# Kernel optimization log

Hardware: AMD Instinct MI355X
Metric: run time of the kernel (lower is better)

Reference implementation:

```python
import jax, jax.numpy as jnp
import numpy as np

MAX_LEN = 200
MAX_K = 3
ITERATION = 3
NEG_PAD = -2.0 ** 16 + 1.0


def setup_inputs() -> dict:
    key = jax.random.key(0)
    k1, k2, k3, k4 = jax.random.split(key, 4)
    B, L, D_in, D_out = 1024, MAX_LEN, 128, 128
    low_capsule = jax.random.normal(k1, (B, L, D_in), dtype=jnp.float32)
    B_matrix = jax.random.normal(k2, (1, MAX_K, L), dtype=jnp.float32)
    S_matrix = jax.random.normal(k3, (D_in, D_out), dtype=jnp.float32)
    # lengths in [1, MAX_LEN]; at least one row hits MAX_LEN so max(seq_len)==MAX_LEN
    seq_len = jax.random.randint(k4, (B, 1), 1, MAX_LEN + 1, dtype=jnp.int64)
    seq_len = seq_len.at[0, 0].set(MAX_LEN)
    return {"low_capsule": low_capsule, "B_matrix": B_matrix,
            "S_matrix": S_matrix, "seq_len": seq_len}


def squash(x):
    # torch code: norm over dim=1 (the capsule axis), keepdim
    sq = jnp.sum(jnp.square(x), axis=1, keepdims=True)
    scale = sq / (1.0 + sq) / jnp.sqrt(sq + 1e-9)
    return scale * x


def reference(low_capsule, B_matrix, S_matrix, seq_len):
    # low_capsule: [B, L, D_in], B_matrix: [1, K, L], S_matrix: [D_in, D_out], seq_len: [B, 1]
    # mask: [B, K, L] (seq_len tiled over K via broadcasting)
    mask = jnp.arange(MAX_LEN)[None, None, :] < seq_len[:, :, None]
    # bilinear projection is loop-invariant (same math as recomputing each iter)
    low_new = jnp.einsum('bld,de->ble', low_capsule, S_matrix)  # [B, L, D_out]
    high = None
    for _ in range(ITERATION):
        logits = jnp.where(mask, B_matrix, jnp.float32(NEG_PAD))  # [B, K, L]
        W = jax.nn.softmax(logits, axis=-1)
        high = squash(jnp.einsum('bkl,ble->bke', W, low_new))  # [B, K, D_out]
        # agreement, summed over batch with keepdim -> [1, K, L]
        B_delta = jnp.einsum('bke,ble->kl', high, low_new)[None]
        B_matrix = B_matrix + B_delta
    return high
```

## Files before the change

### kernel.cpp

```cpp
#include <hip/hip_runtime.h>
#include <math.h>

#define BATCH 1024
#define SEQ   200
#define DIN   128
#define DOUT  128
#define PSTR  608

typedef __attribute__((ext_vector_type(8))) short short8;
typedef __attribute__((ext_vector_type(4))) float f32x4;

__device__ __forceinline__ void async_copy16(const void* g, void* l) {
    __builtin_amdgcn_global_load_lds((const __attribute__((address_space(1))) void*)g,
                                     (__attribute__((address_space(3))) void*)l,
                                     16, 0, 0);
}

__device__ __forceinline__ void split2(float f, short& h, short& l) {
    unsigned u = __float_as_uint(f);
    unsigned r = u + 0x8000u;
    h = (short)(r >> 16);
    float hf = __uint_as_float(r & 0xffff0000u);
    l = (short)(__float_as_uint(f - hf) >> 16);
}

__global__ __launch_bounds__(256) void k_presplit(const float* __restrict__ S,
                                                  short* __restrict__ Sp) {
    int g = blockIdx.x * 256 + threadIdx.x;
    int j = g & 7, lane = (g >> 3) & 63, kt = (g >> 9) & 3, nt = g >> 11;
    int k = kt * 32 + (lane >> 4) * 8 + j;
    int n = nt * 16 + (lane & 15);
    short h, l;
    split2(S[k * DOUT + n], h, l);
    Sp[g] = h;
    Sp[16384 + g] = l;
}

__global__ __launch_bounds__(256, 4) void k_gemm(const float* __restrict__ A,
                                                 const short* __restrict__ Sp,
                                                 float* __restrict__ outn) {
    __shared__ short sSp[16384];
    const int t = threadIdx.x;
    const int w = t >> 6, lane = t & 63;
    const int q = lane >> 4, c = lane & 15;
    const int cg = blockIdx.x & 1;
    const long rowb = (long)(blockIdx.x >> 1) * 128 + w * 32;

    float4 araw[4][2][2];
#pragma unroll
    for (int kt = 0; kt < 4; ++kt)
#pragma unroll
        for (int mt = 0; mt < 2; ++mt) {
            const float* ap = A + (rowb + mt * 16 + c) * DIN + kt * 32 + q * 8;
            araw[kt][mt][0] = *(const float4*)ap;
            araw[kt][mt][1] = *(const float4*)(ap + 4);
        }

#pragma unroll
    for (int i = 0; i < 4; ++i) {
        const int g = w * 4 + i;
        async_copy16(Sp + cg * 8192 + g * 512 + lane * 8, &sSp[g * 512]);
        async_copy16(Sp + 16384 + cg * 8192 + g * 512 + lane * 8, &sSp[8192 + g * 512]);
    }

    short8 ah[4][2], al[4][2];
#pragma unroll
    for (int kt = 0; kt < 4; ++kt)
#pragma unroll
        for (int mt = 0; mt < 2; ++mt) {
            float av[8];
            *(float4*)&av[0] = araw[kt][mt][0];
            *(float4*)&av[4] = araw[kt][mt][1];
#pragma unroll
            for (int j = 0; j < 8; ++j) {
                short h, l;
                split2(av[j], h, l);
                ah[kt][mt][j] = h; al[kt][mt][j] = l;
            }
        }

    f32x4 acc[2][4];
    const f32x4 zz = {0.f, 0.f, 0.f, 0.f};
#pragma unroll
    for (int mt = 0; mt < 2; ++mt)
#pragma unroll
        for (int nt = 0; nt < 4; ++nt) acc[mt][nt] = zz;

    __syncthreads();

#pragma unroll
    for (int kt = 0; kt < 4; ++kt)
#pragma unroll
        for (int nt = 0; nt < 4; ++nt) {
            const int fo = ((nt * 4 + kt) * 64 + lane) * 8;
            short8 sh = *(const short8*)&sSp[fo];
            short8 sl = *(const short8*)&sSp[8192 + fo];
#pragma unroll
            for (int mt = 0; mt < 2; ++mt) {
                acc[mt][nt] = __builtin_amdgcn_mfma_f32_16x16x32_bf16(ah[kt][mt], sh, acc[mt][nt], 0, 0, 0);
                acc[mt][nt] = __builtin_amdgcn_mfma_f32_16x16x32_bf16(al[kt][mt], sh, acc[mt][nt], 0, 0, 0);
                acc[mt][nt] = __builtin_amdgcn_mfma_f32_16x16x32_bf16(ah[kt][mt], sl, acc[mt][nt], 0, 0, 0);
            }
        }
#pragma unroll
    for (int mt = 0; mt < 2; ++mt)
#pragma unroll
        for (int nt = 0; nt < 4; ++nt) {
            const long r0 = rowb + mt * 16 + q * 4;
            const int col = cg * 64 + nt * 16 + c;
#pragma unroll
            for (int r = 0; r < 4; ++r)
                outn[(r0 + r) * DOUT + col] = acc[mt][nt][r];
        }
}

__global__ __launch_bounds__(256, 4) void k_iter(
    const float* __restrict__ lown,
    const float* __restrict__ Bm,
    const int* __restrict__ seq,
    const float* __restrict__ acc0, const float* __restrict__ acc1,
    float* __restrict__ part,
    float* __restrict__ out, int iter) {
    __shared__ float sW[3][SEQ];
    __shared__ f32x4 pBf[815];
    __shared__ float sH[3][64];

    const int t = threadIdx.x, lane = t & 63;
    const int m = t >> 4, cg = t & 15;
    const int b = blockIdx.x >> 1, half = blockIdx.x & 1;
    const float* lp = lown + (size_t)b * (SEQ * DIN) + half * 64;

    float4 dat[13];
#pragma unroll
    for (int i = 0; i < 13; ++i) {
        int r = m + 16 * i;
        int rc = (r < SEQ) ? r : SEQ - 1;
        dat[i] = *(const float4*)(lp + rc * DIN + cg * 4);
    }

    const int n = seq[b];
#pragma unroll
    for (int k = 0; k < 3; ++k) {
        float vv[4], mx = -INFINITY;
#pragma unroll
        for (int i2 = 0; i2 < 4; ++i2) {
            int l = lane + 64 * i2;
            float v = -INFINITY;
            if (l < n) {
                v = Bm[k * SEQ + l];
                if (iter >= 1) v += acc0[k * SEQ + l];
                if (iter >= 2) v += acc1[k * SEQ + l];
            }
            vv[i2] = v;
            mx = fmaxf(mx, v);
        }
        for (int off = 32; off; off >>= 1) mx = fmaxf(mx, __shfl_xor(mx, off, 64));
        float s = 0.f, pv[4];
#pragma unroll
        for (int i2 = 0; i2 < 4; ++i2) {
            pv[i2] = (vv[i2] == -INFINITY) ? 0.f : expf(vv[i2] - mx);
            s += pv[i2];
        }
        for (int off = 32; off; off >>= 1) s += __shfl_xor(s, off, 64);
        float rs = 1.f / s;
#pragma unroll
        for (int i2 = 0; i2 < 4; ++i2) {
            int l = lane + 64 * i2;
            if (l < SEQ) sW[k][l] = pv[i2] * rs;
        }
    }

    f32x4 h0 = {0.f, 0.f, 0.f, 0.f}, h1 = h0, h2 = h0;
#pragma unroll
    for (int i = 0; i < 13; ++i) {
        int r = m + 16 * i;
        if (r < SEQ) {
            float w0 = sW[0][r], w1 = sW[1][r], w2 = sW[2][r];
            f32x4 f = {dat[i].x, dat[i].y, dat[i].z, dat[i].w};
            h0 += w0 * f; h1 += w1 * f; h2 += w2 * f;
        }
    }
    pBf[(m * 3 + 0) * 17 + cg] = h0;
    pBf[(m * 3 + 1) * 17 + cg] = h1;
    pBf[(m * 3 + 2) * 17 + cg] = h2;
    __syncthreads();

    if (t < 64) {
        const int ecg = t >> 2, ej = t & 3;
        float g0 = 0.f, g1 = 0.f, g2 = 0.f;
#pragma unroll
        for (int mm = 0; mm < 16; ++mm) {
            g0 += pBf[(mm * 3 + 0) * 17 + ecg][ej];
            g1 += pBf[(mm * 3 + 1) * 17 + ecg][ej];
            g2 += pBf[(mm * 3 + 2) * 17 + ecg][ej];
        }
        float sq = g0 * g0 + g1 * g1 + g2 * g2;
        float scale = sq / (1.f + sq) / sqrtf(sq + 1e-9f);
        g0 *= scale; g1 *= scale; g2 *= scale;
        if (iter == 2) {
            size_t o = (size_t)b * 3 * DOUT + half * 64 + t;
            out[o] = g0; out[o + DOUT] = g1; out[o + 2 * DOUT] = g2;
        } else {
            sH[0][t] = g0; sH[1][t] = g1; sH[2][t] = g2;
        }
    }
    if (iter == 2) return;
    __syncthreads();

    f32x4 x0 = *(const f32x4*)&sH[0][cg * 4];
    f32x4 x1 = *(const f32x4*)&sH[1][cg * 4];
    f32x4 x2 = *(const f32x4*)&sH[2][cg * 4];
    float* pp = part + (size_t)blockIdx.x * PSTR;
#pragma unroll
    for (int i = 0; i < 13; ++i) {
        int r = m + 16 * i;
        if (r < SEQ) {
            f32x4 f = {dat[i].x, dat[i].y, dat[i].z, dat[i].w};
            f32x4 p0 = x0 * f, p1 = x1 * f, p2 = x2 * f;
            float d0 = p0[0] + p0[1] + p0[2] + p0[3];
            float d1 = p1[0] + p1[1] + p1[2] + p1[3];
            float d2 = p2[0] + p2[1] + p2[2] + p2[3];
#pragma unroll
            for (int off = 1; off < 16; off <<= 1) {
                d0 += __shfl_xor(d0, off, 64);
                d1 += __shfl_xor(d1, off, 64);
                d2 += __shfl_xor(d2, off, 64);
            }
            if (cg == 0) {
                pp[r] = d0; pp[SEQ + r] = d1; pp[2 * SEQ + r] = d2;
            }
        }
    }
}

__global__ __launch_bounds__(256) void k_reduce(const float* __restrict__ part,
                                                float* __restrict__ accN) {
    const int t = threadIdx.x;
    const int r0 = blockIdx.x * 16;
    if (t < 150) {
        float sx = 0.f, sy = 0.f, sz = 0.f, sw = 0.f;
#pragma unroll
        for (int r = 0; r < 16; ++r) {
            float4 v = *(const float4*)&part[(size_t)(r0 + r) * PSTR + t * 4];
            sx += v.x; sy += v.y; sz += v.z; sw += v.w;
        }
        atomicAdd(&accN[4 * t + 0], sx);
        atomicAdd(&accN[4 * t + 1], sy);
        atomicAdd(&accN[4 * t + 2], sz);
        atomicAdd(&accN[4 * t + 3], sw);
    }
}

extern "C" void kernel_launch(void* const* d_in, const int* in_sizes, int n_in,
                              void* d_out, int out_size, void* d_ws, size_t ws_size,
                              hipStream_t stream) {
    const float* low_capsule = (const float*)d_in[0];
    const float* B_matrix    = (const float*)d_in[1];
    const float* S_matrix    = (const float*)d_in[2];
    const int*   seq_len     = (const int*)d_in[3];
    float* out = (float*)d_out;

    float* lown = (float*)d_ws;
    short* Sp   = (short*)(lown + (size_t)BATCH * SEQ * DOUT);
    float* acc0 = (float*)(Sp + 32768);
    float* acc1 = acc0 + 640;
    float* part = acc1 + 640;

    hipMemsetAsync(acc0, 0, 1280 * sizeof(float), stream);

    k_presplit<<<64, 256, 0, stream>>>(S_matrix, Sp);
    k_gemm<<<2 * (BATCH * SEQ) / 128, 256, 0, stream>>>(low_capsule, Sp, lown);

    k_iter<<<2 * BATCH, 256, 0, stream>>>(lown, B_matrix, seq_len, acc0, acc1, part, out, 0);
    k_reduce<<<128, 256, 0, stream>>>(part, acc0);
    k_iter<<<2 * BATCH, 256, 0, stream>>>(lown, B_matrix, seq_len, acc0, acc1, part, out, 1);
    k_reduce<<<128, 256, 0, stream>>>(part, acc1);
    k_iter<<<2 * BATCH, 256, 0, stream>>>(lown, B_matrix, seq_len, acc0, acc1, part, out, 2);
}
```

Baseline: 293.2 us.

## Reassociate projection to skip materializing low_capsule @ S; apply S per batch

Drops the large GEMM that wrote the projected tensor [B,L,128] to workspace. Each iteration now computes W·low on the raw input, multiplies the 3x128 result by S held in shared memory, and projects high back through S^T to get agreement logits. This removes the GEMM and the write and re-read of the large intermediate. In exchange, every block of every iteration reloads S into LDS (64KB) and does a small scalar FMA matvec, and one 512-thread block now covers a whole batch row with occupancy limited by LDS.

Measured after the change: 288.3 us. No clear change (-1.7%).

```diff
diff --git a/kernel.cpp b/kernel.cpp
--- a/kernel.cpp
+++ b/kernel.cpp
@@ -5,130 +5,42 @@
 #define SEQ   200
 #define DIN   128
 #define DOUT  128
+#define SSTR  129
 #define PSTR  608
 
-typedef __attribute__((ext_vector_type(8))) short short8;
 typedef __attribute__((ext_vector_type(4))) float f32x4;
 
-__device__ __forceinline__ void async_copy16(const void* g, void* l) {
-    __builtin_amdgcn_global_load_lds((const __attribute__((address_space(1))) void*)g,
-                                     (__attribute__((address_space(3))) void*)l,
-                                     16, 0, 0);
-}
-
-__device__ __forceinline__ void split2(float f, short& h, short& l) {
-    unsigned u = __float_as_uint(f);
-    unsigned r = u + 0x8000u;
-    h = (short)(r >> 16);
-    float hf = __uint_as_float(r & 0xffff0000u);
-    l = (short)(__float_as_uint(f - hf) >> 16);
-}
-
-__global__ __launch_bounds__(256) void k_presplit(const float* __restrict__ S,
-                                                  short* __restrict__ Sp) {
-    int g = blockIdx.x * 256 + threadIdx.x;
-    int j = g & 7, lane = (g >> 3) & 63, kt = (g >> 9) & 3, nt = g >> 11;
-    int k = kt * 32 + (lane >> 4) * 8 + j;
-    int n = nt * 16 + (lane & 15);
-    short h, l;
-    split2(S[k * DOUT + n], h, l);
-    Sp[g] = h;
-    Sp[16384 + g] = l;
-}
-
-__global__ __launch_bounds__(256, 4) void k_gemm(const float* __restrict__ A,
-                                                 const short* __restrict__ Sp,
-                                                 float* __restrict__ outn) {
-    __shared__ short sSp[16384];
-    const int t = threadIdx.x;
-    const int w = t >> 6, lane = t & 63;
-    const int q = lane >> 4, c = lane & 15;
-    const int cg = blockIdx.x & 1;
-    const long rowb = (long)(blockIdx.x >> 1) * 128 + w * 32;
-
-    float4 araw[4][2][2];
-#pragma unroll
-    for (int kt = 0; kt < 4; ++kt)
-#pragma unroll
-        for (int mt = 0; mt < 2; ++mt) {
-            const float* ap = A + (rowb + mt * 16 + c) * DIN + kt * 32 + q * 8;
-            araw[kt][mt][0] = *(const float4*)ap;
-            araw[kt][mt][1] = *(const float4*)(ap + 4);
-        }
-
-#pragma unroll
-    for (int i = 0; i < 4; ++i) {
-        const int g = w * 4 + i;
-        async_copy16(Sp + cg * 8192 + g * 512 + lane * 8, &sSp[g * 512]);
-        async_copy16(Sp + 16384 + cg * 8192 + g * 512 + lane * 8, &sSp[8192 + g * 512]);
-    }
-
-    short8 ah[4][2], al[4][2];
-#pragma unroll
-    for (int kt = 0; kt < 4; ++kt)
-#pragma unroll
-        for (int mt = 0; mt < 2; ++mt) {
-            float av[8];
-            *(float4*)&av[0] = araw[kt][mt][0];
-            *(float4*)&av[4] = araw[kt][mt][1];
-#pragma unroll
-            for (int j = 0; j < 8; ++j) {
-                short h, l;
-                split2(av[j], h, l);
-                ah[kt][mt][j] = h; al[kt][mt][j] = l;
-            }
-        }
-
-    f32x4 acc[2][4];
-    const f32x4 zz = {0.f, 0.f, 0.f, 0.f};
-#pragma unroll
-    for (int mt = 0; mt < 2; ++mt)
-#pragma unroll
-        for (int nt = 0; nt < 4; ++nt) acc[mt][nt] = zz;
-
-    __syncthreads();
-
-#pragma unroll
-    for (int kt = 0; kt < 4; ++kt)
-#pragma unroll
-        for (int nt = 0; nt < 4; ++nt) {
-            const int fo = ((nt * 4 + kt) * 64 + lane) * 8;
-            short8 sh = *(const short8*)&sSp[fo];
-            short8 sl = *(const short8*)&sSp[8192 + fo];
-#pragma unroll
-            for (int mt = 0; mt < 2; ++mt) {
-                acc[mt][nt] = __builtin_amdgcn_mfma_f32_16x16x32_bf16(ah[kt][mt], sh, acc[mt][nt], 0, 0, 0);
-                acc[mt][nt] = __builtin_amdgcn_mfma_f32_16x16x32_bf16(al[kt][mt], sh, acc[mt][nt], 0, 0, 0);
-                acc[mt][nt] = __builtin_amdgcn_mfma_f32_16x16x32_bf16(ah[kt][mt], sl, acc[mt][nt], 0, 0, 0);
-            }
-        }
-#pragma unroll
-    for (int mt = 0; mt < 2; ++mt)
-#pragma unroll
-        for (int nt = 0; nt < 4; ++nt) {
-            const long r0 = rowb + mt * 16 + q * 4;
-            const int col = cg * 64 + nt * 16 + c;
-#pragma unroll
-            for (int r = 0; r < 4; ++r)
-                outn[(r0 + r) * DOUT + col] = acc[mt][nt][r];
-        }
-}
-
-__global__ __launch_bounds__(256, 4) void k_iter(
-    const float* __restrict__ lown,
+__global__ __launch_bounds__(512, 1) void k_iter(
+    const float* __restrict__ low,
+    const float* __restrict__ S,
     const float* __restrict__ Bm,
     const int* __restrict__ seq,
     const float* __restrict__ acc0, const float* __restrict__ acc1,
     float* __restrict__ part,
     float* __restrict__ out, int iter) {
-    __shared__ float sW[3][SEQ];
-    __shared__ f32x4 pBf[815];
-    __shared__ float sH[3][64];
-
-    const int t = threadIdx.x, lane = t & 63;
-    const int m = t >> 4, cg = t & 15;
-    const int b = blockIdx.x >> 1, half = blockIdx.x & 1;
-    const float* lp = lown + (size_t)b * (SEQ * DIN) + half * 64;
+    __shared__ float sS[128 * SSTR];
+    __shared__ float sW[3 * SEQ];
+    __shared__ f32x4 pY[8][3][32];
+    __shared__ float sY[3 * 128];
+    __shared__ float sHp[3 * 128];
+    __shared__ float sH[3 * 128];
+    __shared__ float sZ[3 * 128];
+
+    const int t = threadIdx.x, lane = t & 63, w = t >> 6;
+    const int m = t >> 5, cg = t & 31;
+    const int b = blockIdx.x;
+    const float* lp = low + (size_t)b * (SEQ * DIN);
+
+    float r0[4], r1[4], r2[4];
+    if (w < 3) {
+#pragma unroll
+        for (int i = 0; i < 4; ++i) {
+            int l = lane + 64 * i; bool inb = l < SEQ;
+            r0[i] = inb ? Bm[w * SEQ + l] : 0.f;
+            r1[i] = (inb && iter >= 1) ? acc0[w * SEQ + l] : 0.f;
+            r2[i] = (inb && iter >= 2) ? acc1[w * SEQ + l] : 0.f;
+        }
+    }
 
     float4 dat[13];
 #pragma unroll
@@ -138,96 +50,133 @@
         dat[i] = *(const float4*)(lp + rc * DIN + cg * 4);
     }
 
-    const int n = seq[b];
-#pragma unroll
-    for (int k = 0; k < 3; ++k) {
-        float vv[4], mx = -INFINITY;
-#pragma unroll
-        for (int i2 = 0; i2 < 4; ++i2) {
-            int l = lane + 64 * i2;
-            float v = -INFINITY;
-            if (l < n) {
-                v = Bm[k * SEQ + l];
-                if (iter >= 1) v += acc0[k * SEQ + l];
-                if (iter >= 2) v += acc1[k * SEQ + l];
-            }
-            vv[i2] = v;
-            mx = fmaxf(mx, v);
+#pragma unroll
+    for (int i = 0; i < 8; ++i) {
+        int g = t + 512 * i;
+        int r = g >> 5, e = (g & 31) * 4;
+        float4 v = *(const float4*)(S + r * DIN + e);
+        sS[r * SSTR + e + 0] = v.x;
+        sS[r * SSTR + e + 1] = v.y;
+        sS[r * SSTR + e + 2] = v.z;
+        sS[r * SSTR + e + 3] = v.w;
+    }
+
+    if (w < 3) {
+        const int n = seq[b];
+        float mx = -INFINITY, vv[4];
+#pragma unroll
+        for (int i = 0; i < 4; ++i) {
+            int l = lane + 64 * i;
+            float v = r0[i] + r1[i] + r2[i];
+            vv[i] = (l < n) ? v : -INFINITY;
+            if (l < n) mx = fmaxf(mx, v);
         }
         for (int off = 32; off; off >>= 1) mx = fmaxf(mx, __shfl_xor(mx, off, 64));
         float s = 0.f, pv[4];
 #pragma unroll
-        for (int i2 = 0; i2 < 4; ++i2) {
-            pv[i2] = (vv[i2] == -INFINITY) ? 0.f : expf(vv[i2] - mx);
-            s += pv[i2];
+        for (int i = 0; i < 4; ++i) {
+            pv[i] = (vv[i] == -INFINITY) ? 0.f : expf(vv[i] - mx);
+            s += pv[i];
         }
         for (int off = 32; off; off >>= 1) s += __shfl_xor(s, off, 64);
         float rs = 1.f / s;
 #pragma unroll
-        for (int i2 = 0; i2 < 4; ++i2) {
-            int l = lane + 64 * i2;
-            if (l < SEQ) sW[k][l] = pv[i2] * rs;
-        }
-    }
-
-    f32x4 h0 = {0.f, 0.f, 0.f, 0.f}, h1 = h0, h2 = h0;
-#pragma unroll
-    for (int i = 0; i < 13; ++i) {
-        int r = m + 16 * i;
-        if (r < SEQ) {
-            float w0 = sW[0][r], w1 = sW[1][r], w2 = sW[2][r];
-            f32x4 f = {dat[i].x, dat[i].y, dat[i].z, dat[i].w};
-            h0 += w0 * f; h1 += w1 * f; h2 += w2 * f;
-        }
-    }
-    pBf[(m * 3 + 0) * 17 + cg] = h0;
-    pBf[(m * 3 + 1) * 17 + cg] = h1;
-    pBf[(m * 3 + 2) * 17 + cg] = h2;
-    __syncthreads();
-
-    if (t < 64) {
-        const int ecg = t >> 2, ej = t & 3;
-        float g0 = 0.f, g1 = 0.f, g2 = 0.f;
-#pragma unroll
-        for (int mm = 0; mm < 16; ++mm) {
-            g0 += pBf[(mm * 3 + 0) * 17 + ecg][ej];
-            g1 += pBf[(mm * 3 + 1) * 17 + ecg][ej];
-            g2 += pBf[(mm * 3 + 2) * 17 + ecg][ej];
-        }
+        for (int i = 0; i < 4; ++i) {
+            int l = lane + 64 * i;
+            if (l < SEQ) sW[w * SEQ + l] = pv[i] * rs;
+        }
+    }
+    __syncthreads();
+
+    {
+        f32x4 h0 = {0.f, 0.f, 0.f, 0.f}, h1 = h0, h2 = h0;
+#pragma unroll
+        for (int i = 0; i < 13; ++i) {
+            int r = m + 16 * i;
+            if (r < SEQ) {
+                float w0 = sW[r], w1 = sW[SEQ + r], w2 = sW[2 * SEQ + r];
+                f32x4 f = {dat[i].x, dat[i].y, dat[i].z, dat[i].w};
+                h0 += w0 * f; h1 += w1 * f; h2 += w2 * f;
+            }
+        }
+#pragma unroll
+        for (int c = 0; c < 4; ++c) {
+            h0[c] += __shfl_xor(h0[c], 32, 64);
+            h1[c] += __shfl_xor(h1[c], 32, 64);
+            h2[c] += __shfl_xor(h2[c], 32, 64);
+        }
+        if (lane < 32) { pY[w][0][cg] = h0; pY[w][1][cg] = h1; pY[w][2][cg] = h2; }
+    }
+    __syncthreads();
+
+    if (t < 384) {
+        const int k = t >> 7, d = t & 127;
+        float yv = 0.f;
+#pragma unroll
+        for (int w8 = 0; w8 < 8; ++w8)
+            yv += pY[w8][k][d >> 2][d & 3];
+        sY[k * 128 + d] = yv;
+    }
+    __syncthreads();
+
+    float hval = 0.f;
+    if (t < 384) {
+        const int k = t >> 7, e = t & 127;
+        float hp = 0.f;
+        for (int d = 0; d < 128; ++d)
+            hp = fmaf(sY[k * 128 + d], sS[d * SSTR + e], hp);
+        hval = hp;
+        sHp[t] = hp;
+    }
+    __syncthreads();
+
+    float scale = 0.f;
+    if (t < 384) {
+        const int e = t & 127;
+        float g0 = sHp[e], g1 = sHp[128 + e], g2 = sHp[256 + e];
         float sq = g0 * g0 + g1 * g1 + g2 * g2;
-        float scale = sq / (1.f + sq) / sqrtf(sq + 1e-9f);
-        g0 *= scale; g1 *= scale; g2 *= scale;
-        if (iter == 2) {
-            size_t o = (size_t)b * 3 * DOUT + half * 64 + t;
-            out[o] = g0; out[o + DOUT] = g1; out[o + 2 * DOUT] = g2;
-        } else {
-            sH[0][t] = g0; sH[1][t] = g1; sH[2][t] = g2;
-        }
-    }
-    if (iter == 2) return;
-    __syncthreads();
-
-    f32x4 x0 = *(const f32x4*)&sH[0][cg * 4];
-    f32x4 x1 = *(const f32x4*)&sH[1][cg * 4];
-    f32x4 x2 = *(const f32x4*)&sH[2][cg * 4];
-    float* pp = part + (size_t)blockIdx.x * PSTR;
-#pragma unroll
-    for (int i = 0; i < 13; ++i) {
-        int r = m + 16 * i;
-        if (r < SEQ) {
-            f32x4 f = {dat[i].x, dat[i].y, dat[i].z, dat[i].w};
-            f32x4 p0 = x0 * f, p1 = x1 * f, p2 = x2 * f;
-            float d0 = p0[0] + p0[1] + p0[2] + p0[3];
-            float d1 = p1[0] + p1[1] + p1[2] + p1[3];
-            float d2 = p2[0] + p2[1] + p2[2] + p2[3];
-#pragma unroll
-            for (int off = 1; off < 16; off <<= 1) {
-                d0 += __shfl_xor(d0, off, 64);
-                d1 += __shfl_xor(d1, off, 64);
-                d2 += __shfl_xor(d2, off, 64);
-            }
-            if (cg == 0) {
-                pp[r] = d0; pp[SEQ + r] = d1; pp[2 * SEQ + r] = d2;
+        scale = sq / (1.f + sq) / sqrtf(sq + 1e-9f);
+    }
+
+    if (iter == 2) {
+        if (t < 384) out[(size_t)b * 384 + t] = hval * scale;
+        return;
+    }
+    if (t < 384) sH[t] = hval * scale;
+    __syncthreads();
+
+    if (t < 384) {
+        const int k = t >> 7, d = t & 127;
+        float zv = 0.f;
+        for (int e = 0; e < 128; ++e)
+            zv = fmaf(sS[d * SSTR + e], sH[k * 128 + e], zv);
+        sZ[k * 128 + d] = zv;
+    }
+    __syncthreads();
+
+    {
+        f32x4 x0 = *(const f32x4*)&sZ[0 * 128 + cg * 4];
+        f32x4 x1 = *(const f32x4*)&sZ[1 * 128 + cg * 4];
+        f32x4 x2 = *(const f32x4*)&sZ[2 * 128 + cg * 4];
+        float* pp = part + (size_t)b * PSTR;
+#pragma unroll
+        for (int i = 0; i < 13; ++i) {
+            int r = m + 16 * i;
+            if (r < SEQ) {
+                f32x4 f = {dat[i].x, dat[i].y, dat[i].z, dat[i].w};
+                f32x4 p0 = x0 * f, p1 = x1 * f, p2 = x2 * f;
+                float d0 = p0[0] + p0[1] + p0[2] + p0[3];
+                float d1 = p1[0] + p1[1] + p1[2] + p1[3];
+                float d2 = p2[0] + p2[1] + p2[2] + p2[3];
+#pragma unroll
+                for (int off = 1; off < 32; off <<= 1) {
+                    d0 += __shfl_xor(d0, off, 64);
+                    d1 += __shfl_xor(d1, off, 64);
+                    d2 += __shfl_xor(d2, off, 64);
+                }
+                if ((lane & 31) == 0) {
+                    pp[r] = d0; pp[SEQ + r] = d1; pp[2 * SEQ + r] = d2;
+                }
             }
         }
     }
@@ -260,20 +209,18 @@
     const int*   seq_len     = (const int*)d_in[3];
     float* out = (float*)d_out;
 
-    float* lown = (float*)d_ws;
-    short* Sp   = (short*)(lown + (size_t)BATCH * SEQ * DOUT);
-    float* acc0 = (float*)(Sp + 32768);
+    float* acc0 = (float*)d_ws;
     float* acc1 = acc0 + 640;
     float* part = acc1 + 640;
 
     hipMemsetAsync(acc0, 0, 1280 * sizeof(float), stream);
 
-    k_presplit<<<64, 256, 0, stream>>>(S_matrix, Sp);
-    k_gemm<<<2 * (BATCH * SEQ) / 128, 256, 0, stream>>>(low_capsule, Sp, lown);
-
-    k_iter<<<2 * BATCH, 256, 0, stream>>>(lown, B_matrix, seq_len, acc0, acc1, part, out, 0);
-    k_reduce<<<128, 256, 0, stream>>>(part, acc0);
-    k_iter<<<2 * BATCH, 256, 0, stream>>>(lown, B_matrix, seq_len, acc0, acc1, part, out, 1);
-    k_reduce<<<128, 256, 0, stream>>>(part, acc1);
-    k_iter<<<2 * BATCH, 256, 0, stream>>>(lown, B_matrix, seq_len, acc0, acc1, part, out, 2);
+    k_iter<<<BATCH, 512, 0, stream>>>(low_capsule, S_matrix, B_matrix, seq_len,
+                                      acc0, acc1, part, out, 0);
+    k_reduce<<<64, 256, 0, stream>>>(part, acc0);
+    k_iter<<<BATCH, 512, 0, stream>>>(low_capsule, S_matrix, B_matrix, seq_len,
+                                      acc0, acc1, part, out, 1);
+    k_reduce<<<64, 256, 0, stream>>>(part, acc1);
+    k_iter<<<BATCH, 512, 0, stream>>>(low_capsule, S_matrix, B_matrix, seq_len,
+                                      acc0, acc1, part, out, 2);
 }
```
